# Performance work log

Measured on AMD Instinct MI355X. Metric: run time of the kernel, lower is better.

## Reference

```python
import jax, jax.numpy as jnp
import numpy as np

NUM_RELATIONS = 3
NUM_HEADS = 1

N_NODES = 50000
N_EDGES = 300000
D = 256  # in_channels == out_channels == out_channels*num_heads
W_SCALE = 0.02  # realistic init scale; keeps linear-attention normalizer dominated by N_r


def setup_inputs() -> dict:
    key = jax.random.key(0)
    k = jax.random.split(key, 7)
    x = jax.random.normal(k[0], (N_NODES, D), dtype=jnp.float32)
    Wq = jax.random.normal(k[1], (NUM_RELATIONS, D, D * NUM_HEADS), dtype=jnp.float32) * W_SCALE
    Wk = jax.random.normal(k[2], (NUM_RELATIONS, D, D * NUM_HEADS), dtype=jnp.float32) * W_SCALE
    Wv = jax.random.normal(k[3], (NUM_RELATIONS, D, D * NUM_HEADS), dtype=jnp.float32) * W_SCALE
    Whp = jax.random.normal(k[4], (D * NUM_HEADS, D), dtype=jnp.float32) * W_SCALE
    edge_index = jax.random.randint(k[5], (2, N_EDGES), 0, N_NODES, dtype=jnp.int64)
    edge_type = jax.random.randint(k[6], (N_EDGES,), 0, NUM_RELATIONS, dtype=jnp.int64)
    return {"x": x, "Wq": Wq, "Wk": Wk, "Wv": Wv, "Whp": Whp,
            "edge_index": edge_index, "edge_type": edge_type}


def _trans_conv(x, Wq, Wk, Wv, Whp, edge_index, edge_type):
    # x: [N, F], Wq/Wk/Wv: [R, F, H*Dh], Whp: [H*Dh, Dh], edge_index: [2, E]
    row, col = edge_index[0], edge_index[1]
    N = x.shape[0]
    R = Wq.shape[0]
    H = NUM_HEADS
    Dh = Wq.shape[-1] // H
    xr = x[row]  # [E, F] gathered source-node features
    xc = x[col]  # [E, F] gathered target-node features
    x_out = jnp.zeros((N, Dh), dtype=x.dtype)
    for r in range(R):  # small fixed relation loop (structurally distinct weights)
        m = (edge_type == r).astype(x.dtype)  # [E] relation mask (handles ragged sizes)
        Nr = jnp.sum(m)  # number of edges of this relation (the 'N' in full_attention_conv)
        q = (xr @ Wq[r]).reshape(-1, H, Dh)  # [E, H, Dh]
        kk = (xc @ Wk[r]).reshape(-1, H, Dh)
        v = (xc @ Wv[r]).reshape(-1, H, Dh)
        # linear attention (no softmax), masked so only relation-r edges contribute
        kvs = jnp.einsum('e,ehm,ehd->hmd', m, kk, v)        # [H, Dh, Dh]
        num = jnp.einsum('ehm,hmd->ehd', q, kvs) + Nr * v    # [E, H, Dh]
        ks_sum = jnp.einsum('e,ehm->hm', m, kk)              # [H, Dh]
        norm = jnp.einsum('ehm,hm->eh', q, ks_sum)[..., None] + Nr  # [E, H, 1]
        attn = (num / norm).mean(axis=1)                     # [E, Dh] (mean over heads)
        x_out = x_out.at[row].add(m[:, None] * attn)         # scatter-add to source nodes
    return x_out @ Whp  # head projection


def reference(x, Wq, Wk, Wv, Whp, edge_index, edge_type):
    return _trans_conv(x, Wq, Wk, Wv, Whp, edge_index, edge_type)
```

## Files before the change

### kernel.cpp

```cpp
#include <hip/hip_runtime.h>

#define NN 50000
#define EE 300000
#define DD 256
#define RR 3
#define NPAD 50048
#define GS 64
#define SCT (RR * NN)
#define SCB 1024
#define SNB ((SCT + SCB - 1) / SCB)
#define TBLK 3128

using bf16x8 = __attribute__((ext_vector_type(8))) short;
using f32x4  = __attribute__((ext_vector_type(4))) float;

__device__ __forceinline__ float bf2f(unsigned short u) {
    return __uint_as_float(((unsigned)u) << 16);
}
__device__ __forceinline__ unsigned short f2bf(float f) {
    unsigned u = __float_as_uint(f);
    return (unsigned short)((u + 0x7fffu + ((u >> 16) & 1u)) >> 16);
}
__device__ __forceinline__ void gload_lds16(const void* g, void* l) {
    __builtin_amdgcn_global_load_lds(
        (const __attribute__((address_space(1))) unsigned int*)g,
        (__attribute__((address_space(3))) unsigned int*)l, 16, 0, 0);
}

__global__ __launch_bounds__(256) void prep_tc(
    const float* __restrict__ x, const float* __restrict__ Wq,
    const float* __restrict__ Wk, const float* __restrict__ Wv,
    const float* __restrict__ Whp,
    unsigned short* __restrict__ xb, unsigned short* __restrict__ xT,
    unsigned short* __restrict__ Wqb, unsigned short* __restrict__ Wkb,
    unsigned short* __restrict__ Wvb, unsigned short* __restrict__ WhpT)
{
    const int tid = threadIdx.x;
    if (blockIdx.x < TBLK) {
        __shared__ unsigned short t[64][66];
        const int tb = blockIdx.x;
        const int n0 = (tb % 782) * 64, i0 = (tb / 782) * 64;
        const int nl = tid >> 2, c0 = (tid & 3) * 16;
        unsigned short vb[16];
        int n = n0 + nl;
        if (n < NN) {
            const float* src = x + (size_t)n * DD + i0 + c0;
#pragma unroll
            for (int q = 0; q < 16; q += 4) {
                float4 v = *(const float4*)(src + q);
                vb[q] = f2bf(v.x); vb[q + 1] = f2bf(v.y);
                vb[q + 2] = f2bf(v.z); vb[q + 3] = f2bf(v.w);
            }
#pragma unroll
            for (int q = 0; q < 16; q += 4)
                *(ushort4*)(xb + (size_t)n * DD + i0 + c0 + q) =
                    make_ushort4(vb[q], vb[q + 1], vb[q + 2], vb[q + 3]);
        } else {
#pragma unroll
            for (int q = 0; q < 16; q++) vb[q] = 0;
        }
#pragma unroll
        for (int q = 0; q < 16; q++) t[nl][c0 + q] = vb[q];
        __syncthreads();
        const int il = tid >> 2, nc0 = (tid & 3) * 16;
        unsigned short ob[16];
#pragma unroll
        for (int q = 0; q < 16; q++) ob[q] = t[nc0 + q][il];
#pragma unroll
        for (int q = 0; q < 16; q += 4)
            *(ushort4*)(xT + (size_t)(i0 + il) * NPAD + n0 + nc0 + q) =
                make_ushort4(ob[q], ob[q + 1], ob[q + 2], ob[q + 3]);
    } else {
        int t = (blockIdx.x - TBLK) * 256 + tid;
        int slot = t >> 16, o = t & 65535;
        int a = o >> 8, b = o & 255;
        if (slot < 3)       Wqb[(size_t)slot * 65536 + o] = f2bf(Wq[(size_t)slot * 65536 + o]);
        else if (slot < 6)  Wkb[(size_t)(slot - 3) * 65536 + o] = f2bf(Wk[(size_t)(slot - 3) * 65536 + o]);
        else if (slot < 9)  Wvb[(size_t)(slot - 6) * 65536 + o] = f2bf(Wv[(size_t)(slot - 6) * 65536 + o]);
        else if (slot == 9) WhpT[o] = f2bf(Whp[b * 256 + a]);
    }
}

__global__ __launch_bounds__(256) void count_kernel(
    const int* __restrict__ erow, const int* __restrict__ ecol,
    const int* __restrict__ etype, int* __restrict__ c_in,
    int* __restrict__ c_out, int* __restrict__ nr)
{
    __shared__ int lnr[RR];
    if (threadIdx.x < RR) lnr[threadIdx.x] = 0;
    __syncthreads();
    int g = blockIdx.x * blockDim.x + threadIdx.x;
    int stride = gridDim.x * blockDim.x;
    for (int e = g; e < EE; e += stride) {
        int t = etype[e];
        atomicAdd(&c_out[t * NN + erow[e]], 1);
        atomicAdd(&c_in[t * NN + ecol[e]], 1);
        atomicAdd(&lnr[t], 1);
    }
    __syncthreads();
    if (threadIdx.x < RR) atomicAdd(&nr[threadIdx.x], lnr[threadIdx.x]);
}

__global__ __launch_bounds__(256) void scan_reduce(
    const int* __restrict__ cnt, int* __restrict__ bsum)
{
    __shared__ int ws[4];
    const int b = blockIdx.x, tid = threadIdx.x;
    const int i = b * SCB + tid * 4;
    int s = 0;
    if (i < SCT) {
        int4 v = *(const int4*)(cnt + i);
        s = v.x + v.y + v.z + v.w;
    }
#pragma unroll
    for (int off = 32; off; off >>= 1) s += __shfl_down(s, off, 64);
    if ((tid & 63) == 0) ws[tid >> 6] = s;
    __syncthreads();
    if (tid == 0) bsum[b] = ws[0] + ws[1] + ws[2] + ws[3];
}

__global__ __launch_bounds__(256) void scan_top(
    const int* __restrict__ bsum, int* __restrict__ boff, int* __restrict__ offT)
{
    __shared__ int bs[256];
    const int tid = threadIdx.x;
    int v = tid < SNB ? bsum[tid] : 0;
    bs[tid] = v;
    __syncthreads();
    for (int d = 1; d < 256; d <<= 1) {
        int t = (tid >= d) ? bs[tid - d] : 0;
        __syncthreads();
        bs[tid] += t;
        __syncthreads();
    }
    if (tid < SNB) boff[tid] = tid ? bs[tid - 1] : 0;
    if (tid == 255) *offT = bs[255];
}

__global__ __launch_bounds__(256) void scan_bot(
    const int* __restrict__ cnt, const int* __restrict__ boff,
    int* __restrict__ off, int* __restrict__ cur)
{
    __shared__ int bs[256];
    const int b = blockIdx.x, tid = threadIdx.x;
    const int i = b * SCB + tid * 4;
    int4 v = make_int4(0, 0, 0, 0);
    if (i < SCT) v = *(const int4*)(cnt + i);
    int s = v.x + v.y + v.z + v.w;
    bs[tid] = s;
    __syncthreads();
    for (int d = 1; d < 256; d <<= 1) {
        int t = (tid >= d) ? bs[tid - d] : 0;
        __syncthreads();
        bs[tid] += t;
        __syncthreads();
    }
    if (i < SCT) {
        int pre = boff[b] + (tid ? bs[tid - 1] : 0);
        int4 o;
        o.x = pre;
        o.y = pre + v.x;
        o.z = pre + v.x + v.y;
        o.w = pre + v.x + v.y + v.z;
        *(int4*)(off + i) = o;
        *(int4*)(cur + i) = o;
    }
}

__global__ __launch_bounds__(256) void fill_kernel(
    const int* __restrict__ erow, const int* __restrict__ ecol,
    const int* __restrict__ etype, int* __restrict__ cur,
    int* __restrict__ scol)
{
    int e = blockIdx.x * 256 + threadIdx.x;
    if (e < EE) {
        int key = etype[e] * NN + erow[e];
        int p = atomicAdd(&cur[key], 1);
        scol[p] = ecol[e];
    }
}

__global__ __launch_bounds__(256) void wbfxw_kernel(
    const unsigned short* __restrict__ xT, const int* __restrict__ c_in,
    float* __restrict__ xw, unsigned short* __restrict__ wbf)
{
    const int tid = threadIdx.x;
    if (blockIdx.x < 256) {
        __shared__ float red[3][4];
        const int i = blockIdx.x;
        float a0 = 0.f, a1 = 0.f, a2 = 0.f;
        for (int n = tid * 4; n < NN; n += 1024) {
            ushort4 xv = *(const ushort4*)(xT + (size_t)i * NPAD + n);
            int4 w0 = *(const int4*)(c_in + n);
            int4 w1 = *(const int4*)(c_in + NN + n);
            int4 w2 = *(const int4*)(c_in + 2 * NN + n);
            float f0 = bf2f(xv.x), f1 = bf2f(xv.y), f2 = bf2f(xv.z), f3 = bf2f(xv.w);
            a0 += f0 * w0.x + f1 * w0.y + f2 * w0.z + f3 * w0.w;
            a1 += f0 * w1.x + f1 * w1.y + f2 * w1.z + f3 * w1.w;
            a2 += f0 * w2.x + f1 * w2.y + f2 * w2.z + f3 * w2.w;
        }
#pragma unroll
        for (int off = 32; off; off >>= 1) {
            a0 += __shfl_down(a0, off, 64);
            a1 += __shfl_down(a1, off, 64);
            a2 += __shfl_down(a2, off, 64);
        }
        if ((tid & 63) == 0) {
            red[0][tid >> 6] = a0; red[1][tid >> 6] = a1; red[2][tid >> 6] = a2;
        }
        __syncthreads();
        if (tid < 3)
            xw[tid * 256 + i] = red[tid][0] + red[tid][1] + red[tid][2] + red[tid][3];
    } else {
        int t = (blockIdx.x - 256) * 256 + tid;
        if (t < 3 * NPAD) {
            int r = t / NPAD, n = t % NPAD;
            wbf[t] = f2bf(n < NN ? (float)c_in[r * NN + n] : 0.f);
        }
    }
}

__global__ __launch_bounds__(512) void g_kernel(
    const unsigned short* __restrict__ xT, const unsigned short* __restrict__ wbf,
    float* __restrict__ Gp)
{
    __shared__ __align__(16) char ldsA[16384];
    __shared__ __align__(16) char ldsB[16384];
    const int tid = threadIdx.x, lane = tid & 63, wid = tid >> 6;
    const int wr = wid >> 1, wc = wid & 1;
    const int i0 = blockIdx.x * 128, j0 = blockIdx.y * 128;
    const int TPZ = (NPAD / 64 + GS - 1) / GS;
    const int kt0 = blockIdx.z * TPZ;
    const int kt1 = min(NPAD / 64, kt0 + TPZ);

    f32x4 acc[3][2][4];
#pragma unroll
    for (int r = 0; r < 3; r++)
#pragma unroll
        for (int m = 0; m < 2; m++)
#pragma unroll
            for (int n = 0; n < 4; n++) acc[r][m][n] = (f32x4){0.f, 0.f, 0.f, 0.f};

    for (int kt = kt0; kt < kt1; kt++) {
        const int kbyte = kt * 128;
#pragma unroll
        for (int is = 0; is < 2; is++) {
            int lb = is * 8192 + wid * 1024;
            int d = lb + lane * 16;
            int row = d >> 7;
            int sc_ = (d & 127) ^ ((row & 7) << 4);
            gload_lds16((const char*)xT + (size_t)(i0 + row) * (NPAD * 2) + kbyte + sc_, ldsA + lb);
            gload_lds16((const char*)xT + (size_t)(j0 + row) * (NPAD * 2) + kbyte + sc_, ldsB + lb);
        }
        __syncthreads();
#pragma unroll
        for (int kk = 0; kk < 2; kk++) {
            const int cb = kk * 64 + ((lane >> 4) << 4);
            bf16x8 bfr[4];
#pragma unroll
            for (int n = 0; n < 4; n++) {
                int rn = wc * 64 + n * 16 + (lane & 15);
                bfr[n] = *(const bf16x8*)(ldsB + rn * 128 + (cb ^ ((rn & 7) << 4)));
            }
            float au[2][8];
#pragma unroll
            for (int m = 0; m < 2; m++) {
                int row = wr * 32 + m * 16 + (lane & 15);
                bf16x8 ar = *(const bf16x8*)(ldsA + row * 128 + (cb ^ ((row & 7) << 4)));
#pragma unroll
                for (int q = 0; q < 8; q++) au[m][q] = bf2f((unsigned short)ar[q]);
            }
            const int nb = kt * 64 + kk * 32 + ((lane >> 4) << 3);
#pragma unroll
            for (int r = 0; r < 3; r++) {
                bf16x8 wv = *(const bf16x8*)(wbf + (size_t)r * NPAD + nb);
                float wf[8];
#pragma unroll
                for (int q = 0; q < 8; q++) wf[q] = bf2f((unsigned short)wv[q]);
                bf16x8 am[2];
#pragma unroll
                for (int m = 0; m < 2; m++)
#pragma unroll
                    for (int q = 0; q < 8; q++)
                        am[m][q] = (short)f2bf(au[m][q] * wf[q]);
#pragma unroll
                for (int m = 0; m < 2; m++)
#pragma unroll
                    for (int n = 0; n < 4; n++)
                        acc[r][m][n] = __builtin_amdgcn_mfma_f32_16x16x32_bf16(
                            am[m], bfr[n], acc[r][m][n], 0, 0, 0);
            }
        }
        __syncthreads();
    }
    float* base = Gp + ((size_t)blockIdx.z * 4 + blockIdx.x * 2 + blockIdx.y) * 3 * 16384;
#pragma unroll
    for (int r = 0; r < 3; r++)
#pragma unroll
        for (int m = 0; m < 2; m++)
#pragma unroll
            for (int n = 0; n < 4; n++) {
                int col = wc * 64 + n * 16 + (lane & 15);
                int rw0 = wr * 32 + m * 16 + ((lane >> 4) << 2);
#pragma unroll
                for (int reg = 0; reg < 4; reg++)
                    base[r * 16384 + (rw0 + reg) * 128 + col] = acc[r][m][n][reg];
            }
}

__global__ __launch_bounds__(256) void greduce_kernel(
    const float* __restrict__ Gp, unsigned short* __restrict__ Gb)
{
    int gid = blockIdx.x * 256 + threadIdx.x;
    int t = gid >> 14, rem = gid & 16383;
    int r = t % 3, tile = t / 3;
    float s = 0.f;
    for (int z = 0; z < GS; z++)
        s += Gp[(size_t)z * 196608 + ((size_t)tile * 3 + r) * 16384 + rem];
    int i = (tile >> 1) * 128 + (rem >> 7);
    int j = (tile & 1) * 128 + (rem & 127);
    Gb[(size_t)r * 65536 + i * 256 + j] = f2bf(s);
}

__global__ __launch_bounds__(256) void matvec_bf(
    const unsigned short* __restrict__ Mat, const float* __restrict__ v,
    float* __restrict__ y)
{
    __shared__ float vs[256];
    const int b = blockIdx.x;
    const int r = b >> 6, rb = (b & 63) * 4;
    const int tid = threadIdx.x;
    vs[tid] = v[r * 256 + tid];
    __syncthreads();
    const int wid = tid >> 6, lane = tid & 63;
    const int row = rb + wid;
    ushort4 m4 = *(const ushort4*)(Mat + (size_t)r * 65536 + row * 256 + lane * 4);
    float s = bf2f(m4.x) * vs[lane * 4] + bf2f(m4.y) * vs[lane * 4 + 1] +
              bf2f(m4.z) * vs[lane * 4 + 2] + bf2f(m4.w) * vs[lane * 4 + 3];
#pragma unroll
    for (int off = 32; off; off >>= 1) s += __shfl_down(s, off, 64);
    if (lane == 0) y[r * 256 + row] = s;
}

__global__ __launch_bounds__(256) void gather_kernel(
    const unsigned short* __restrict__ xb, const int* __restrict__ scol,
    const int* __restrict__ off, const float* __restrict__ tv,
    const int* __restrict__ c_out, const int* __restrict__ nr,
    unsigned short* __restrict__ Ascat, float* __restrict__ s2g)
{
    __shared__ float ts[768];
    __shared__ float nrs[RR];
    const int tid = threadIdx.x;
    for (int k = tid; k < 768; k += 256) ts[k] = tv[k];
    if (tid < RR) nrs[tid] = (float)nr[tid];
    __syncthreads();
    const int wid = tid >> 6, lane = tid & 63;
    const int n = blockIdx.x * 4 + wid;
    if (n >= NN) return;
    ushort4 xv = *(const ushort4*)(xb + (size_t)n * DD + lane * 4);
    float xf[4] = {bf2f(xv.x), bf2f(xv.y), bf2f(xv.z), bf2f(xv.w)};
    float dots[RR];
#pragma unroll
    for (int t = 0; t < RR; t++) {
        float s = xf[0] * ts[t * 256 + lane * 4] + xf[1] * ts[t * 256 + lane * 4 + 1] +
                  xf[2] * ts[t * 256 + lane * 4 + 2] + xf[3] * ts[t * 256 + lane * 4 + 3];
#pragma unroll
        for (int o = 32; o; o >>= 1) s += __shfl_xor(s, o, 64);
        dots[t] = s;
    }
#pragma unroll
    for (int t = 0; t < RR; t++) {
        float nrf = nrs[t];
        float denom = dots[t] + nrf;
        if (lane == 0) {
            int cnt = c_out[t * NN + n];
            s2g[(size_t)t * NN + n] = cnt ? (float)cnt / denom : 0.f;
        }
        float acc[4] = {0.f, 0.f, 0.f, 0.f};
        int b0 = off[t * NN + n], b1 = off[t * NN + n + 1];
        for (int i = b0; i < b1; i++) {
            int col = scol[i];
            ushort4 v = *(const ushort4*)(xb + (size_t)col * DD + lane * 4);
            acc[0] += bf2f(v.x); acc[1] += bf2f(v.y);
            acc[2] += bf2f(v.z); acc[3] += bf2f(v.w);
        }
        float s1 = nrf / denom;
        ushort4 o2;
        o2.x = f2bf(s1 * acc[0]); o2.y = f2bf(s1 * acc[1]);
        o2.z = f2bf(s1 * acc[2]); o2.w = f2bf(s1 * acc[3]);
        *(ushort4*)(Ascat + (size_t)n * 768 + t * 256 + lane * 4) = o2;
    }
}

template <int MODE, int SWZ>
__global__ __launch_bounds__(256) void gemm_nt(
    const unsigned short* __restrict__ A, int lda,
    const unsigned short* __restrict__ B, int ldb,
    void* __restrict__ Cv, int ldc, int M, int KK,
    size_t sa, size_t sb, size_t sc)
{
    A += (size_t)blockIdx.z * sa;
    B += (size_t)blockIdx.z * sb;
    __shared__ __align__(16) char ldsA[16384];
    __shared__ __align__(16) char ldsB[16384];
    const int tid = threadIdx.x, lane = tid & 63, wid = tid >> 6;
    const int wr = wid >> 1, wc = wid & 1;
    int bx = blockIdx.x;
    if (SWZ) {
        int nwg = gridDim.x, q = nwg >> 3, rem = nwg & 7;
        int xcd = bx & 7, idx = bx >> 3;
        bx = (xcd < rem ? xcd * (q + 1) : rem * (q + 1) + (xcd - rem) * q) + idx;
    }
    const int row0 = bx * 128, col0 = blockIdx.y * 128;

    f32x4 acc[4][4];
#pragma unroll
    for (int m = 0; m < 4; m++)
#pragma unroll
        for (int n = 0; n < 4; n++) acc[m][n] = (f32x4){0.f, 0.f, 0.f, 0.f};

    for (int k0 = 0; k0 < KK; k0 += 64) {
#pragma unroll
        for (int is = 0; is < 4; is++) {
            int lb = is * 4096 + wid * 1024;
            int d = lb + lane * 16;
            int row = d >> 7;
            int sc_ = (d & 127) ^ ((row & 7) << 4);
            int gr = row0 + row; gr = gr < M ? gr : M - 1;
            gload_lds16((const char*)(A + (size_t)gr * lda + k0) + sc_, ldsA + lb);
            int rn = col0 + row;
            gload_lds16((const char*)(B + (size_t)rn * ldb + k0) + sc_, ldsB + lb);
        }
        __syncthreads();
#pragma unroll
        for (int kk = 0; kk < 2; kk++) {
            bf16x8 af[4], bf_[4];
            const int cb = kk * 64 + ((lane >> 4) << 4);
#pragma unroll
            for (int m = 0; m < 4; m++) {
                int row = wr * 64 + m * 16 + (lane & 15);
                af[m] = *(const bf16x8*)(ldsA + row * 128 + (cb ^ ((row & 7) << 4)));
                int rn = wc * 64 + m * 16 + (lane & 15);
                bf_[m] = *(const bf16x8*)(ldsB + rn * 128 + (cb ^ ((rn & 7) << 4)));
            }
#pragma unroll
            for (int m = 0; m < 4; m++)
#pragma unroll
                for (int n = 0; n < 4; n++)
                    acc[m][n] = __builtin_amdgcn_mfma_f32_16x16x32_bf16(
                        af[m], bf_[n], acc[m][n], 0, 0, 0);
        }
        __syncthreads();
    }

#pragma unroll
    for (int m = 0; m < 4; m++) {
#pragma unroll
        for (int reg = 0; reg < 4; reg++) {
            int r = row0 + wr * 64 + m * 16 + ((lane >> 4) << 2) + reg;
            if (r >= M) continue;
#pragma unroll
            for (int n = 0; n < 4; n++) {
                int c = col0 + wc * 64 + n * 16 + (lane & 15);
                float v = acc[m][n][reg];
                if (MODE == 0)
                    ((unsigned short*)Cv)[(size_t)blockIdx.z * sc + (size_t)r * ldc + c] = f2bf(v);
                else
                    ((float*)Cv)[(size_t)blockIdx.z * sc + (size_t)r * ldc + c] = v;
            }
        }
    }
}

__global__ __launch_bounds__(512) void gemm_big(
    const unsigned short* __restrict__ Xb, const unsigned short* __restrict__ As,
    const unsigned short* __restrict__ Bm, const float* __restrict__ s2g,
    float* __restrict__ C, int M)
{
    extern __shared__ __align__(16) char lds[];
    char* ldsA = lds;
    char* ldsB = lds + 32768;
    float* s2l = (float*)(lds + 98304);
    const int tid = threadIdx.x, lane = tid & 63, wid = tid >> 6;
    const int wr = wid >> 2, wc = wid & 3;
    int bx = blockIdx.x;
    {
        int nwg = gridDim.x, q = nwg >> 3, rem = nwg & 7;
        int xcd = bx & 7, idx = bx >> 3;
        bx = (xcd < rem ? xcd * (q + 1) : rem * (q + 1) + (xcd - rem) * q) + idx;
    }
    const int row0 = bx * 128;

    if (tid < 384) {
        int rsel = tid >> 7, rr = tid & 127;
        int gr = row0 + rr; gr = gr < M ? gr : M - 1;
        s2l[tid] = s2g[(size_t)rsel * NN + gr];
    }

    f32x4 accO[4][4], acc[4][4];
#pragma unroll
    for (int m = 0; m < 4; m++)
#pragma unroll
        for (int n = 0; n < 4; n++) {
            accO[m][n] = (f32x4){0.f, 0.f, 0.f, 0.f};
            acc[m][n]  = (f32x4){0.f, 0.f, 0.f, 0.f};
        }

#define STAGE_A(buf, Asrc, ldaE, kE)                                           \
    { _Pragma("unroll")                                                        \
      for (int is = 0; is < 2; is++) {                                         \
          int lb = is * 8192 + wid * 1024;                                     \
          int d = lb + lane * 16;                                              \
          int row = d >> 7;                                                    \
          int sc_ = (d & 127) ^ ((row & 7) << 4);                              \
          int gr = row0 + row; gr = gr < M ? gr : M - 1;                       \
          gload_lds16((const char*)((Asrc) + (size_t)gr * (ldaE) + (kE)) + sc_,\
                      ldsA + (buf) * 16384 + lb); } }

#define STAGE_B(buf, kE)                                                       \
    { _Pragma("unroll")                                                        \
      for (int is = 0; is < 4; is++) {                                         \
          int lb = is * 8192 + wid * 1024;                                     \
          int d = lb + lane * 16;                                              \
          int row = d >> 7;                                                    \
          int sc_ = (d & 127) ^ ((row & 7) << 4);                              \
          gload_lds16((const char*)(Bm + (size_t)row * 1536 + (kE)) + sc_,     \
                      ldsB + (buf) * 32768 + lb); } }

#define MFMA_STEP(abuf, bbuf, ACC)                                             \
    { const char* bA = ldsA + (abuf) * 16384;                                  \
      const char* bB = ldsB + (bbuf) * 32768;                                  \
      _Pragma("unroll")                                                        \
      for (int kk = 0; kk < 2; kk++) {                                         \
          bf16x8 af[4], bf_[4];                                                \
          const int cb = kk * 64 + ((lane >> 4) << 4);                         \
          _Pragma("unroll")                                                    \
          for (int m = 0; m < 4; m++) {                                        \
              int row = wr * 64 + m * 16 + (lane & 15);                        \
              af[m] = *(const bf16x8*)(bA + row * 128 + (cb ^ ((row & 7) << 4)));\
              int rn = wc * 64 + m * 16 + (lane & 15);                         \
              bf_[m] = *(const bf16x8*)(bB + rn * 128 + (cb ^ ((rn & 7) << 4)));\
          }                                                                    \
          _Pragma("unroll")                                                    \
          for (int m = 0; m < 4; m++)                                          \
              _Pragma("unroll")                                                \
              for (int n = 0; n < 4; n++)                                      \
                  ACC[m][n] = __builtin_amdgcn_mfma_f32_16x16x32_bf16(         \
                      af[m], bf_[n], ACC[m][n], 0, 0, 0); } }

    STAGE_A(0, Xb, 256, 0);
    STAGE_B(0, 0);
    __syncthreads();
    int ab = 0, bb = 0;

    for (int r = 0; r < 3; r++) {
        for (int kt = 0; kt < 4; kt++) {
            if (kt < 3)      { STAGE_A(ab ^ 1, Xb, 256, (kt + 1) * 64);
                               STAGE_B(bb ^ 1, r * 256 + (kt + 1) * 64); }
            else if (r < 2)  { STAGE_A(ab ^ 1, Xb, 256, 0);
                               STAGE_B(bb ^ 1, (r + 1) * 256); }
            else             { STAGE_A(ab ^ 1, As, 768, 0);
                               STAGE_B(bb ^ 1, 768); }
            MFMA_STEP(ab, bb, acc);
            __syncthreads();
            ab ^= 1; bb ^= 1;
        }
#pragma unroll
        for (int m = 0; m < 4; m++) {
            f32x4 sv = *(const f32x4*)&s2l[r * 128 + wr * 64 + m * 16 + ((lane >> 4) << 2)];
#pragma unroll
            for (int n = 0; n < 4; n++) {
                accO[m][n] += sv * acc[m][n];
                acc[m][n] = (f32x4){0.f, 0.f, 0.f, 0.f};
            }
        }
    }
    for (int st = 0; st < 12; st++) {
        if (st < 11) { STAGE_A(ab ^ 1, As, 768, (st + 1) * 64);
                       STAGE_B(bb ^ 1, 768 + (st + 1) * 64); }
        MFMA_STEP(ab, bb, accO);
        __syncthreads();
        ab ^= 1; bb ^= 1;
    }
#undef STAGE_A
#undef STAGE_B
#undef MFMA_STEP

#pragma unroll
    for (int m = 0; m < 4; m++) {
#pragma unroll
        for (int reg = 0; reg < 4; reg++) {
            int r = row0 + wr * 64 + m * 16 + ((lane >> 4) << 2) + reg;
            if (r >= M) continue;
#pragma unroll
            for (int n = 0; n < 4; n++) {
                int c = wc * 64 + n * 16 + (lane & 15);
                C[(size_t)r * 256 + c] = accO[m][n][reg];
            }
        }
    }
}

extern "C" void kernel_launch(void* const* d_in, const int* in_sizes, int n_in,
                              void* d_out, int out_size, void* d_ws, size_t ws_size,
                              hipStream_t stream)
{
    const float* x   = (const float*)d_in[0];
    const float* Wq  = (const float*)d_in[1];
    const float* Wk  = (const float*)d_in[2];
    const float* Wv  = (const float*)d_in[3];
    const float* Whp = (const float*)d_in[4];
    const int* eidx  = (const int*)d_in[5];
    const int* etyp  = (const int*)d_in[6];
    const int* erow = eidx;
    const int* ecol = eidx + EE;
    float* out = (float*)d_out;

    char* p = (char*)d_ws;
    unsigned short* xb    = (unsigned short*)p; p += (size_t)NN * DD * 2;
    unsigned short* xT    = (unsigned short*)p; p += (size_t)DD * NPAD * 2;
    char*           regB  = p;                  p += (size_t)NN * 768 * 2;
    unsigned short* Gb    = (unsigned short*)p; p += (size_t)RR * 65536 * 2;
    unsigned short* M1    = (unsigned short*)p; p += (size_t)RR * 65536 * 2;
    unsigned short* Tm    = (unsigned short*)p; p += (size_t)RR * 65536 * 2;
    unsigned short* Bout  = (unsigned short*)p; p += (size_t)256 * 1536 * 2;
    unsigned short* Wqb   = (unsigned short*)p; p += (size_t)RR * 65536 * 2;
    unsigned short* Wkb   = (unsigned short*)p; p += (size_t)RR * 65536 * 2;
    unsigned short* Wvb   = (unsigned short*)p; p += (size_t)RR * 65536 * 2;
    unsigned short* WhpT  = (unsigned short*)p; p += 65536 * 2;
    unsigned short* wbf   = (unsigned short*)p; p += (size_t)RR * NPAD * 2;
    float*          xw    = (float*)p;          p += 768 * 4;
    float*          tv    = (float*)p;          p += 768 * 4;
    float*          s2g   = (float*)p;          p += (size_t)RR * NN * 4;
    int*            c_in  = (int*)p;            p += (size_t)RR * NN * 4;
    int*            c_out = (int*)p;            p += (size_t)RR * NN * 4;
    int*            nr    = (int*)p;            p += 4 * 4;
    int*            off   = (int*)p;            p += (size_t)(RR * NN + 4) * 4;
    int*            cur   = (int*)p;            p += (size_t)RR * NN * 4;
    int*            scol  = (int*)p;            p += (size_t)EE * 4;
    int*            bsum  = (int*)p;            p += SNB * 4;
    int*            boff  = (int*)p;            p += SNB * 4;
    float*          Gp    = (float*)regB;
    unsigned short* Ascat = (unsigned short*)regB;

    hipFuncSetAttribute((const void*)gemm_big,
                        hipFuncAttributeMaxDynamicSharedMemorySize, 99840);

    prep_tc<<<TBLK + 2560, 256, 0, stream>>>(x, Wq, Wk, Wv, Whp, xb, xT, Wqb, Wkb, Wvb, WhpT);
    hipMemsetAsync(c_in, 0, (size_t)(6 * NN + 4) * sizeof(int), stream);
    count_kernel<<<512, 256, 0, stream>>>(erow, ecol, etyp, c_in, c_out, nr);
    scan_reduce<<<SNB, 256, 0, stream>>>(c_out, bsum);
    scan_top<<<1, 256, 0, stream>>>(bsum, boff, off + SCT);
    scan_bot<<<SNB, 256, 0, stream>>>(c_out, boff, off, cur);
    fill_kernel<<<(EE + 255) / 256, 256, 0, stream>>>(erow, ecol, etyp, cur, scol);
    wbfxw_kernel<<<256 + (3 * NPAD + 255) / 256, 256, 0, stream>>>(xT, c_in, xw, wbf);

    gemm_nt<0, 0><<<dim3(2, 2, 3), 256, 0, stream>>>(Wqb, 256, Wkb, 256, M1, 256, 256, 256,
                                                     65536, 65536, 65536);
    gemm_nt<0, 0><<<dim3(2, 2, 3), 256, 0, stream>>>(WhpT, 256, Wvb, 256, Bout + 768, 1536,
                                                     256, 256, 0, 65536, 256);

    g_kernel<<<dim3(2, 2, GS), 512, 0, stream>>>(xT, wbf, Gp);
    greduce_kernel<<<12 * 64, 256, 0, stream>>>(Gp, Gb);

    gemm_nt<0, 0><<<dim3(2, 2, 3), 256, 0, stream>>>(M1, 256, Gb, 256, Tm, 256, 256, 256,
                                                     65536, 65536, 65536);
    gemm_nt<0, 0><<<dim3(2, 2, 3), 256, 0, stream>>>(Bout + 768, 1536, Tm, 256, Bout, 1536,
                                                     256, 256, 256, 65536, 256);
    matvec_bf<<<192, 256, 0, stream>>>(M1, xw, tv);

    gather_kernel<<<(NN + 3) / 4, 256, 0, stream>>>(xb, scol, off, tv, c_out, nr, Ascat, s2g);

    const int MB2 = (NN + 127) / 128;
    gemm_big<<<dim3(MB2, 1), 512, 99840, stream>>>(xb, Ascat, Bout, s2g, out, NN);
}
```

Measured before the change: 292.4 us.

## Merge prep kernels, split gather into per-segment sums, scale in GEMM epilogue

Folds the edge counting into the prep kernel and the scan-reduce into the xw/wbf kernel, and merges scan_top into scan_bot, which cuts several launches. The gather kernel is split into independent per-(relation,node) segment-sum waves plus a separate scale computation. The s1 scaling moves from the gather output into the big GEMM's per-relation accumulation through a unified 24-step loop. This raises parallelism in the gather and removes serial launches, at the cost of extra LDS, an extra s1g buffer, and more epilogue scaling work in the GEMM.

```diff
diff --git a/kernel.cpp b/kernel.cpp
--- a/kernel.cpp
+++ b/kernel.cpp
@@ -10,6 +10,9 @@
 #define SCB 1024
 #define SNB ((SCT + SCB - 1) / SCB)
 #define TBLK 3128
+#define WBLK 2560
+#define CBLK 512
+#define SBLK 12500
 
 using bf16x8 = __attribute__((ext_vector_type(8))) short;
 using f32x4  = __attribute__((ext_vector_type(4))) float;
@@ -33,7 +36,10 @@
     const float* __restrict__ Whp,
     unsigned short* __restrict__ xb, unsigned short* __restrict__ xT,
     unsigned short* __restrict__ Wqb, unsigned short* __restrict__ Wkb,
-    unsigned short* __restrict__ Wvb, unsigned short* __restrict__ WhpT)
+    unsigned short* __restrict__ Wvb, unsigned short* __restrict__ WhpT,
+    const int* __restrict__ erow, const int* __restrict__ ecol,
+    const int* __restrict__ etype, int* __restrict__ c_in,
+    int* __restrict__ c_out, int* __restrict__ nr)
 {
     const int tid = threadIdx.x;
     if (blockIdx.x < TBLK) {
@@ -70,7 +76,7 @@
         for (int q = 0; q < 16; q += 4)
             *(ushort4*)(xT + (size_t)(i0 + il) * NPAD + n0 + nc0 + q) =
                 make_ushort4(ob[q], ob[q + 1], ob[q + 2], ob[q + 3]);
-    } else {
+    } else if (blockIdx.x < TBLK + WBLK) {
         int t = (blockIdx.x - TBLK) * 256 + tid;
         int slot = t >> 16, o = t & 65535;
         int a = o >> 8, b = o & 255;
@@ -78,116 +84,45 @@
         else if (slot < 6)  Wkb[(size_t)(slot - 3) * 65536 + o] = f2bf(Wk[(size_t)(slot - 3) * 65536 + o]);
         else if (slot < 9)  Wvb[(size_t)(slot - 6) * 65536 + o] = f2bf(Wv[(size_t)(slot - 6) * 65536 + o]);
         else if (slot == 9) WhpT[o] = f2bf(Whp[b * 256 + a]);
-    }
-}
-
-__global__ __launch_bounds__(256) void count_kernel(
-    const int* __restrict__ erow, const int* __restrict__ ecol,
-    const int* __restrict__ etype, int* __restrict__ c_in,
-    int* __restrict__ c_out, int* __restrict__ nr)
-{
-    __shared__ int lnr[RR];
-    if (threadIdx.x < RR) lnr[threadIdx.x] = 0;
-    __syncthreads();
-    int g = blockIdx.x * blockDim.x + threadIdx.x;
-    int stride = gridDim.x * blockDim.x;
-    for (int e = g; e < EE; e += stride) {
-        int t = etype[e];
-        atomicAdd(&c_out[t * NN + erow[e]], 1);
-        atomicAdd(&c_in[t * NN + ecol[e]], 1);
-        atomicAdd(&lnr[t], 1);
-    }
-    __syncthreads();
-    if (threadIdx.x < RR) atomicAdd(&nr[threadIdx.x], lnr[threadIdx.x]);
-}
-
-__global__ __launch_bounds__(256) void scan_reduce(
-    const int* __restrict__ cnt, int* __restrict__ bsum)
-{
-    __shared__ int ws[4];
-    const int b = blockIdx.x, tid = threadIdx.x;
-    const int i = b * SCB + tid * 4;
-    int s = 0;
-    if (i < SCT) {
-        int4 v = *(const int4*)(cnt + i);
-        s = v.x + v.y + v.z + v.w;
-    }
-#pragma unroll
-    for (int off = 32; off; off >>= 1) s += __shfl_down(s, off, 64);
-    if ((tid & 63) == 0) ws[tid >> 6] = s;
-    __syncthreads();
-    if (tid == 0) bsum[b] = ws[0] + ws[1] + ws[2] + ws[3];
-}
-
-__global__ __launch_bounds__(256) void scan_top(
-    const int* __restrict__ bsum, int* __restrict__ boff, int* __restrict__ offT)
-{
-    __shared__ int bs[256];
-    const int tid = threadIdx.x;
-    int v = tid < SNB ? bsum[tid] : 0;
-    bs[tid] = v;
-    __syncthreads();
-    for (int d = 1; d < 256; d <<= 1) {
-        int t = (tid >= d) ? bs[tid - d] : 0;
-        __syncthreads();
-        bs[tid] += t;
-        __syncthreads();
-    }
-    if (tid < SNB) boff[tid] = tid ? bs[tid - 1] : 0;
-    if (tid == 255) *offT = bs[255];
-}
-
-__global__ __launch_bounds__(256) void scan_bot(
-    const int* __restrict__ cnt, const int* __restrict__ boff,
-    int* __restrict__ off, int* __restrict__ cur)
-{
-    __shared__ int bs[256];
-    const int b = blockIdx.x, tid = threadIdx.x;
-    const int i = b * SCB + tid * 4;
-    int4 v = make_int4(0, 0, 0, 0);
-    if (i < SCT) v = *(const int4*)(cnt + i);
-    int s = v.x + v.y + v.z + v.w;
-    bs[tid] = s;
-    __syncthreads();
-    for (int d = 1; d < 256; d <<= 1) {
-        int t = (tid >= d) ? bs[tid - d] : 0;
-        __syncthreads();
-        bs[tid] += t;
-        __syncthreads();
-    }
-    if (i < SCT) {
-        int pre = boff[b] + (tid ? bs[tid - 1] : 0);
-        int4 o;
-        o.x = pre;
-        o.y = pre + v.x;
-        o.z = pre + v.x + v.y;
-        o.w = pre + v.x + v.y + v.z;
-        *(int4*)(off + i) = o;
-        *(int4*)(cur + i) = o;
-    }
-}
-
-__global__ __launch_bounds__(256) void fill_kernel(
-    const int* __restrict__ erow, const int* __restrict__ ecol,
-    const int* __restrict__ etype, int* __restrict__ cur,
-    int* __restrict__ scol)
-{
-    int e = blockIdx.x * 256 + threadIdx.x;
-    if (e < EE) {
-        int key = etype[e] * NN + erow[e];
-        int p = atomicAdd(&cur[key], 1);
-        scol[p] = ecol[e];
-    }
-}
-
-__global__ __launch_bounds__(256) void wbfxw_kernel(
+    } else {
+        __shared__ int lnr[RR];
+        if (tid < RR) lnr[tid] = 0;
+        __syncthreads();
+        int cb = blockIdx.x - (TBLK + WBLK);
+        for (int e = cb * 256 + tid; e < EE; e += CBLK * 256) {
+            int t = etype[e];
+            atomicAdd(&c_out[t * NN + erow[e]], 1);
+            atomicAdd(&c_in[t * NN + ecol[e]], 1);
+            atomicAdd(&lnr[t], 1);
+        }
+        __syncthreads();
+        if (tid < RR) atomicAdd(&nr[tid], lnr[tid]);
+    }
+}
+
+__global__ __launch_bounds__(256) void prep2(
+    const int* __restrict__ c_out, int* __restrict__ bsum,
     const unsigned short* __restrict__ xT, const int* __restrict__ c_in,
     float* __restrict__ xw, unsigned short* __restrict__ wbf)
 {
     const int tid = threadIdx.x;
-    if (blockIdx.x < 256) {
+    if (blockIdx.x < SNB) {
+        __shared__ int ws[4];
+        const int b = blockIdx.x;
+        const int i = b * SCB + tid * 4;
+        int s = 0;
+        if (i < SCT) {
+            int4 v = *(const int4*)(c_out + i);
+            s = v.x + v.y + v.z + v.w;
+        }
+#pragma unroll
+        for (int off = 32; off; off >>= 1) s += __shfl_down(s, off, 64);
+        if ((tid & 63) == 0) ws[tid >> 6] = s;
+        __syncthreads();
+        if (tid == 0) bsum[b] = ws[0] + ws[1] + ws[2] + ws[3];
+    } else if (blockIdx.x < SNB + 256) {
         __shared__ float red[3][4];
-        const int i = blockIdx.x;
+        const int i = blockIdx.x - SNB;
         float a0 = 0.f, a1 = 0.f, a2 = 0.f;
         for (int n = tid * 4; n < NN; n += 1024) {
             ushort4 xv = *(const ushort4*)(xT + (size_t)i * NPAD + n);
@@ -212,11 +147,66 @@
         if (tid < 3)
             xw[tid * 256 + i] = red[tid][0] + red[tid][1] + red[tid][2] + red[tid][3];
     } else {
-        int t = (blockIdx.x - 256) * 256 + tid;
+        int t = (blockIdx.x - SNB - 256) * 256 + tid;
         if (t < 3 * NPAD) {
             int r = t / NPAD, n = t % NPAD;
             wbf[t] = f2bf(n < NN ? (float)c_in[r * NN + n] : 0.f);
         }
+    }
+}
+
+__global__ __launch_bounds__(256) void scan_bot(
+    const int* __restrict__ cnt, const int* __restrict__ bsum,
+    int* __restrict__ off, int* __restrict__ cur)
+{
+    __shared__ int bs[256], loc[256];
+    const int b = blockIdx.x, tid = threadIdx.x;
+    int v = tid < SNB ? bsum[tid] : 0;
+    bs[tid] = v;
+    __syncthreads();
+    for (int d = 1; d < 256; d <<= 1) {
+        int t = (tid >= d) ? bs[tid - d] : 0;
+        __syncthreads();
+        bs[tid] += t;
+        __syncthreads();
+    }
+    const int myboff = b ? bs[b - 1] : 0;
+    const int total = bs[255];
+    const int i = b * SCB + tid * 4;
+    int4 vv = make_int4(0, 0, 0, 0);
+    if (i < SCT) vv = *(const int4*)(cnt + i);
+    int s = vv.x + vv.y + vv.z + vv.w;
+    loc[tid] = s;
+    __syncthreads();
+    for (int d = 1; d < 256; d <<= 1) {
+        int t = (tid >= d) ? loc[tid - d] : 0;
+        __syncthreads();
+        loc[tid] += t;
+        __syncthreads();
+    }
+    if (i < SCT) {
+        int pre = myboff + (tid ? loc[tid - 1] : 0);
+        int4 o;
+        o.x = pre;
+        o.y = pre + vv.x;
+        o.z = pre + vv.x + vv.y;
+        o.w = pre + vv.x + vv.y + vv.z;
+        *(int4*)(off + i) = o;
+        *(int4*)(cur + i) = o;
+    }
+    if (b == 0 && tid == 0) off[SCT] = total;
+}
+
+__global__ __launch_bounds__(256) void fill_kernel(
+    const int* __restrict__ erow, const int* __restrict__ ecol,
+    const int* __restrict__ etype, int* __restrict__ cur,
+    int* __restrict__ scol)
+{
+    int e = blockIdx.x * 256 + threadIdx.x;
+    if (e < EE) {
+        int key = etype[e] * NN + erow[e];
+        int p = atomicAdd(&cur[key], 1);
+        scol[p] = ecol[e];
     }
 }
 
@@ -342,53 +332,53 @@
     if (lane == 0) y[r * 256 + row] = s;
 }
 
-__global__ __launch_bounds__(256) void gather_kernel(
+__global__ __launch_bounds__(256) void sssum_kernel(
     const unsigned short* __restrict__ xb, const int* __restrict__ scol,
     const int* __restrict__ off, const float* __restrict__ tv,
     const int* __restrict__ c_out, const int* __restrict__ nr,
-    unsigned short* __restrict__ Ascat, float* __restrict__ s2g)
-{
-    __shared__ float ts[768];
-    __shared__ float nrs[RR];
+    unsigned short* __restrict__ Sraw, float* __restrict__ s1g,
+    float* __restrict__ s2g)
+{
     const int tid = threadIdx.x;
-    for (int k = tid; k < 768; k += 256) ts[k] = tv[k];
-    if (tid < RR) nrs[tid] = (float)nr[tid];
-    __syncthreads();
     const int wid = tid >> 6, lane = tid & 63;
-    const int n = blockIdx.x * 4 + wid;
-    if (n >= NN) return;
-    ushort4 xv = *(const ushort4*)(xb + (size_t)n * DD + lane * 4);
-    float xf[4] = {bf2f(xv.x), bf2f(xv.y), bf2f(xv.z), bf2f(xv.w)};
-    float dots[RR];
-#pragma unroll
-    for (int t = 0; t < RR; t++) {
-        float s = xf[0] * ts[t * 256 + lane * 4] + xf[1] * ts[t * 256 + lane * 4 + 1] +
-                  xf[2] * ts[t * 256 + lane * 4 + 2] + xf[3] * ts[t * 256 + lane * 4 + 3];
-#pragma unroll
-        for (int o = 32; o; o >>= 1) s += __shfl_xor(s, o, 64);
-        dots[t] = s;
-    }
-#pragma unroll
-    for (int t = 0; t < RR; t++) {
-        float nrf = nrs[t];
-        float denom = dots[t] + nrf;
-        if (lane == 0) {
-            int cnt = c_out[t * NN + n];
-            s2g[(size_t)t * NN + n] = cnt ? (float)cnt / denom : 0.f;
-        }
-        float acc[4] = {0.f, 0.f, 0.f, 0.f};
-        int b0 = off[t * NN + n], b1 = off[t * NN + n + 1];
+    if (blockIdx.x < SBLK) {
+        __shared__ float ts[768];
+        __shared__ float nrs[RR];
+        for (int k = tid; k < 768; k += 256) ts[k] = tv[k];
+        if (tid < RR) nrs[tid] = (float)nr[tid];
+        __syncthreads();
+        const int n = blockIdx.x * 4 + wid;
+        if (n >= NN) return;
+        ushort4 xv = *(const ushort4*)(xb + (size_t)n * DD + lane * 4);
+        float xf[4] = {bf2f(xv.x), bf2f(xv.y), bf2f(xv.z), bf2f(xv.w)};
+#pragma unroll
+        for (int t = 0; t < RR; t++) {
+            float s = xf[0] * ts[t * 256 + lane * 4] + xf[1] * ts[t * 256 + lane * 4 + 1] +
+                      xf[2] * ts[t * 256 + lane * 4 + 2] + xf[3] * ts[t * 256 + lane * 4 + 3];
+#pragma unroll
+            for (int o = 32; o; o >>= 1) s += __shfl_xor(s, o, 64);
+            if (lane == 0) {
+                float nrf = nrs[t];
+                float denom = s + nrf;
+                int cnt = c_out[t * NN + n];
+                s2g[(size_t)t * NN + n] = cnt ? (float)cnt / denom : 0.f;
+                s1g[(size_t)t * NN + n] = nrf / denom;
+            }
+        }
+    } else {
+        int seg = (blockIdx.x - SBLK) * 4 + wid;
+        if (seg >= SCT) return;
+        int b0 = off[seg], b1 = off[seg + 1];
+        float a0 = 0.f, a1 = 0.f, a2 = 0.f, a3 = 0.f;
         for (int i = b0; i < b1; i++) {
             int col = scol[i];
             ushort4 v = *(const ushort4*)(xb + (size_t)col * DD + lane * 4);
-            acc[0] += bf2f(v.x); acc[1] += bf2f(v.y);
-            acc[2] += bf2f(v.z); acc[3] += bf2f(v.w);
-        }
-        float s1 = nrf / denom;
-        ushort4 o2;
-        o2.x = f2bf(s1 * acc[0]); o2.y = f2bf(s1 * acc[1]);
-        o2.z = f2bf(s1 * acc[2]); o2.w = f2bf(s1 * acc[3]);
-        *(ushort4*)(Ascat + (size_t)n * 768 + t * 256 + lane * 4) = o2;
+            a0 += bf2f(v.x); a1 += bf2f(v.y); a2 += bf2f(v.z); a3 += bf2f(v.w);
+        }
+        int t = seg / NN, n = seg - t * NN;
+        ushort4 o;
+        o.x = f2bf(a0); o.y = f2bf(a1); o.z = f2bf(a2); o.w = f2bf(a3);
+        *(ushort4*)(Sraw + (size_t)n * 768 + t * 256 + lane * 4) = o;
     }
 }
 
@@ -473,14 +463,14 @@
 }
 
 __global__ __launch_bounds__(512) void gemm_big(
-    const unsigned short* __restrict__ Xb, const unsigned short* __restrict__ As,
+    const unsigned short* __restrict__ Xb, const unsigned short* __restrict__ Sraw,
     const unsigned short* __restrict__ Bm, const float* __restrict__ s2g,
-    float* __restrict__ C, int M)
+    const float* __restrict__ s1g, float* __restrict__ C, int M)
 {
     extern __shared__ __align__(16) char lds[];
     char* ldsA = lds;
     char* ldsB = lds + 32768;
-    float* s2l = (float*)(lds + 98304);
+    float* sl  = (float*)(lds + 98304);
     const int tid = threadIdx.x, lane = tid & 63, wid = tid >> 6;
     const int wr = wid >> 2, wc = wid & 3;
     int bx = blockIdx.x;
@@ -491,10 +481,10 @@
     }
     const int row0 = bx * 128;
 
-    if (tid < 384) {
-        int rsel = tid >> 7, rr = tid & 127;
+    for (int k = tid; k < 768; k += 512) {
+        int pp = k >> 7, rr = k & 127;
         int gr = row0 + rr; gr = gr < M ? gr : M - 1;
-        s2l[tid] = s2g[(size_t)rsel * NN + gr];
+        sl[k] = pp < 3 ? s2g[(size_t)pp * NN + gr] : s1g[(size_t)(pp - 3) * NN + gr];
     }
 
     f32x4 accO[4][4], acc[4][4];
@@ -553,34 +543,28 @@
     __syncthreads();
     int ab = 0, bb = 0;
 
-    for (int r = 0; r < 3; r++) {
-        for (int kt = 0; kt < 4; kt++) {
-            if (kt < 3)      { STAGE_A(ab ^ 1, Xb, 256, (kt + 1) * 64);
-                               STAGE_B(bb ^ 1, r * 256 + (kt + 1) * 64); }
-            else if (r < 2)  { STAGE_A(ab ^ 1, Xb, 256, 0);
-                               STAGE_B(bb ^ 1, (r + 1) * 256); }
-            else             { STAGE_A(ab ^ 1, As, 768, 0);
-                               STAGE_B(bb ^ 1, 768); }
-            MFMA_STEP(ab, bb, acc);
-            __syncthreads();
-            ab ^= 1; bb ^= 1;
-        }
-#pragma unroll
-        for (int m = 0; m < 4; m++) {
-            f32x4 sv = *(const f32x4*)&s2l[r * 128 + wr * 64 + m * 16 + ((lane >> 4) << 2)];
-#pragma unroll
-            for (int n = 0; n < 4; n++) {
-                accO[m][n] += sv * acc[m][n];
-                acc[m][n] = (f32x4){0.f, 0.f, 0.f, 0.f};
-            }
-        }
-    }
-    for (int st = 0; st < 12; st++) {
-        if (st < 11) { STAGE_A(ab ^ 1, As, 768, (st + 1) * 64);
-                       STAGE_B(bb ^ 1, 768 + (st + 1) * 64); }
-        MFMA_STEP(ab, bb, accO);
+    for (int st = 0; st < 24; st++) {
+        if (st < 23) {
+            int nst = st + 1;
+            if (nst < 12) { STAGE_A(ab ^ 1, Xb, 256, (nst & 3) * 64); }
+            else          { STAGE_A(ab ^ 1, Sraw, 768, (nst - 12) * 64); }
+            STAGE_B(bb ^ 1, nst * 64);
+        }
+        MFMA_STEP(ab, bb, acc);
         __syncthreads();
         ab ^= 1; bb ^= 1;
+        if ((st & 3) == 3) {
+            int pp = st >> 2;
+#pragma unroll
+            for (int m = 0; m < 4; m++) {
+                f32x4 sv = *(const f32x4*)&sl[pp * 128 + wr * 64 + m * 16 + ((lane >> 4) << 2)];
+#pragma unroll
+                for (int n = 0; n < 4; n++) {
+                    accO[m][n] += sv * acc[m][n];
+                    acc[m][n] = (f32x4){0.f, 0.f, 0.f, 0.f};
+                }
+            }
+        }
     }
 #undef STAGE_A
 #undef STAGE_B
@@ -632,6 +616,7 @@
     float*          xw    = (float*)p;          p += 768 * 4;
     float*          tv    = (float*)p;          p += 768 * 4;
     float*          s2g   = (float*)p;          p += (size_t)RR * NN * 4;
+    float*          s1g   = (float*)p;          p += (size_t)RR * NN * 4;
     int*            c_in  = (int*)p;            p += (size_t)RR * NN * 4;
     int*            c_out = (int*)p;            p += (size_t)RR * NN * 4;
     int*            nr    = (int*)p;            p += 4 * 4;
@@ -639,21 +624,20 @@
     int*            cur   = (int*)p;            p += (size_t)RR * NN * 4;
     int*            scol  = (int*)p;            p += (size_t)EE * 4;
     int*            bsum  = (int*)p;            p += SNB * 4;
-    int*            boff  = (int*)p;            p += SNB * 4;
     float*          Gp    = (float*)regB;
-    unsigned short* Ascat = (unsigned short*)regB;
+    unsigned short* Sraw  = (unsigned short*)regB;
 
     hipFuncSetAttribute((const void*)gemm_big,
-                        hipFuncAttributeMaxDynamicSharedMemorySize, 99840);
-
-    prep_tc<<<TBLK + 2560, 256, 0, stream>>>(x, Wq, Wk, Wv, Whp, xb, xT, Wqb, Wkb, Wvb, WhpT);
+                        hipFuncAttributeMaxDynamicSharedMemorySize, 101376);
+
     hipMemsetAsync(c_in, 0, (size_t)(6 * NN + 4) * sizeof(int), stream);
-    count_kernel<<<512, 256, 0, stream>>>(erow, ecol, etyp, c_in, c_out, nr);
-    scan_reduce<<<SNB, 256, 0, stream>>>(c_out, bsum);
-    scan_top<<<1, 256, 0, stream>>>(bsum, boff, off + SCT);
-    scan_bot<<<SNB, 256, 0, stream>>>(c_out, boff, off, cur);
+    prep_tc<<<TBLK + WBLK + CBLK, 256, 0, stream>>>(
+        x, Wq, Wk, Wv, Whp, xb, xT, Wqb, Wkb, Wvb, WhpT,
+        erow, ecol, etyp, c_in, c_out, nr);
+    prep2<<<SNB + 256 + (3 * NPAD + 255) / 256, 256, 0, stream>>>(
+        c_out, bsum, xT, c_in, xw, wbf);
+    scan_bot<<<SNB, 256, 0, stream>>>(c_out, bsum, off, cur);
     fill_kernel<<<(EE + 255) / 256, 256, 0, stream>>>(erow, ecol, etyp, cur, scol);
-    wbfxw_kernel<<<256 + (3 * NPAD + 255) / 256, 256, 0, stream>>>(xT, c_in, xw, wbf);
 
     gemm_nt<0, 0><<<dim3(2, 2, 3), 256, 0, stream>>>(Wqb, 256, Wkb, 256, M1, 256, 256, 256,
                                                      65536, 65536, 65536);
@@ -669,8 +653,9 @@
                                                      256, 256, 256, 65536, 256);
     matvec_bf<<<192, 256, 0, stream>>>(M1, xw, tv);
 
-    gather_kernel<<<(NN + 3) / 4, 256, 0, stream>>>(xb, scol, off, tv, c_out, nr, Ascat, s2g);
+    sssum_kernel<<<SBLK + (SCT + 3) / 4, 256, 0, stream>>>(
+        xb, scol, off, tv, c_out, nr, Sraw, s1g, s2g);
 
     const int MB2 = (NN + 127) / 128;
-    gemm_big<<<dim3(MB2, 1), 512, 99840, stream>>>(xb, Ascat, Bout, s2g, out, NN);
-}
+    gemm_big<<<dim3(MB2, 1), 512, 101376, stream>>>(xb, Sraw, Bout, s2g, s1g, out, NN);
+}
```

New measurement: 310.3 us. 6.1% more time.
